# Kernel tuning notes

Hardware: AMD Instinct MI355X
Metric: run time of the kernel (lower is better)

The kernel has to match this reference:

```python
import jax, jax.numpy as jnp
import numpy as np

B, S, D, H, F = 4, 2048, 1024, 16, 4096
HD = D // H
EPS = 1e-5


def _xavier(key, shape, fan_in, fan_out):
    a = float(np.sqrt(6.0 / (fan_in + fan_out)))
    return jax.random.uniform(key, shape, jnp.float32, -a, a)


def setup_inputs() -> dict:
    key = jax.random.key(0)
    ks = jax.random.split(key, 8)
    x = jax.random.normal(ks[0], (B, S, D), jnp.float32)
    # torch xavier_uniform on (1,H,D,HD) uses fan_in=D, fan_out=HD
    Wq = _xavier(ks[1], (H, D, HD), D, HD)
    Wk = _xavier(ks[2], (H, D, HD), D, HD)
    Wv = _xavier(ks[3], (H, D, HD), D, HD)
    Wo = _xavier(ks[4], (D, D), D, D)
    w_in = _xavier(ks[5], (D, F), D, F)
    b_in = jnp.zeros((F,), jnp.float32)
    w_out = _xavier(ks[6], (F, D), F, D)
    b_out = jnp.zeros((D,), jnp.float32)
    g1 = jnp.ones((D,), jnp.float32)
    be1 = jnp.zeros((D,), jnp.float32)
    g2 = jnp.ones((D,), jnp.float32)
    be2 = jnp.zeros((D,), jnp.float32)
    return {"x": x, "Wq": Wq, "Wk": Wk, "Wv": Wv, "Wo": Wo,
            "g1": g1, "be1": be1, "w_in": w_in, "b_in": b_in,
            "w_out": w_out, "b_out": b_out, "g2": g2, "be2": be2}


def _layernorm(x, g, b):
    mu = jnp.mean(x, axis=-1, keepdims=True)
    var = jnp.mean(jnp.square(x - mu), axis=-1, keepdims=True)
    return (x - mu) * jax.lax.rsqrt(var + EPS) * g + b


def reference(x, Wq, Wk, Wv, Wo, g1, be1, w_in, b_in, w_out, b_out, g2, be2):
    b, s, d = x.shape
    h, _, hd = Wq.shape
    q = jnp.einsum('bsd,hde->bhse', x, Wq)
    k = jnp.einsum('bsd,hde->bhse', x, Wk)
    v = jnp.einsum('bsd,hde->bhse', x, Wv)
    scores = jnp.einsum('bhse,bhte->bhst', q, k) / jnp.sqrt(jnp.float32(hd))
    causal = jnp.triu(jnp.ones((s, s), bool), k=1)  # [S,S]
    scores = jnp.where(causal, -jnp.inf, scores)
    p = jax.nn.softmax(scores, axis=-1)
    attn = jnp.einsum('bhst,bhte->bhse', p, v)
    # torch .view on contiguous (B,H,S,hd) -> (B,S,H*hd): plain reshape (no transpose)
    attn = attn.reshape(b, s, h * hd)
    attn = attn @ Wo
    x = _layernorm(x + attn, g1, be1)
    ffn = jax.nn.relu(x @ w_in + b_in) @ w_out + b_out
    x = _layernorm(x + ffn, g2, be2)
    return x
```

## Files before the change

### kernel.cpp

```cpp
#include <hip/hip_runtime.h>
#include <hip/hip_bf16.h>

typedef __hip_bfloat16 bf16;

#define BB 4
#define SS 2048
#define DD 1024
#define HH 16
#define FF 4096
#define HD 64
#define LN_EPS 1e-5f
#define QSCALE 0.1803368801111204f

typedef __attribute__((ext_vector_type(8))) __bf16 bf16x8;
typedef __attribute__((ext_vector_type(8))) unsigned short u16x8;
typedef __attribute__((ext_vector_type(4))) float f32x4;

__device__ __forceinline__ float cvt(float v) { return v; }
__device__ __forceinline__ float cvt(bf16 v) { return __bfloat162float(v); }
__device__ __forceinline__ void stf(float* p, float v) { *p = v; }
__device__ __forceinline__ void stf(bf16* p, float v) { *p = __float2bfloat16(v); }

__device__ __forceinline__ unsigned short f2bf_rne(float x) {
    unsigned int u = __float_as_uint(x);
    unsigned int r = (u + 0x7fffu + ((u >> 16) & 1u)) >> 16;
    return (unsigned short)r;
}

__device__ __forceinline__ void async_cp16(const void* g, void* l) {
    __builtin_amdgcn_global_load_lds(
        (const __attribute__((address_space(1))) unsigned int*)g,
        (__attribute__((address_space(3))) unsigned int*)l, 16, 0, 0);
}

template <int N>
__device__ __forceinline__ void s_wait_vmcnt() {
    asm volatile("s_waitcnt vmcnt(%0)" ::"n"(N) : "memory");
    __builtin_amdgcn_sched_barrier(0);
}

__device__ __forceinline__ void sync_raw() {
    asm volatile("" ::: "memory");
    __builtin_amdgcn_s_barrier();
    asm volatile("" ::: "memory");
    __builtin_amdgcn_sched_barrier(0);
}

template <int EPI, int BW>
__device__ __forceinline__ void gemm_body(
        const bf16* __restrict__ A, const bf16* __restrict__ Bt,
        bf16* __restrict__ C, const float* __restrict__ bias,
        const bf16* __restrict__ resb,
        bf16* __restrict__ C2, bf16* __restrict__ C3,
        int M, int N, int K, float oscale) {
    __shared__ unsigned short As[128 * 64];
    __shared__ unsigned short Bs[128 * 64];

    const int tid = threadIdx.x;
    const int lane = tid & 63;
    const int w = tid >> 6;
    const int wm = w >> 1, wn = w & 1;

    const int gx = gridDim.x, gy = gridDim.y;
    const int id = blockIdx.y * gx + blockIdx.x;
    const int R = gy >> 3;
    const int k = id & 7;
    const int j = id >> 3;
    const int sbs = R * BW;
    const int sb = j / sbs;
    const int rem = j % sbs;
    const int by = k * R + rem / BW;
    const int bx = sb * BW + rem % BW;
    const int m0 = by * 128, n0 = bx * 128;

    int ff[4], fr[4], fg[4];
#pragma unroll
    for (int i = 0; i < 4; ++i) {
        ff[i] = tid + i * 256;
        fr[i] = ff[i] >> 3;
        fg[i] = (ff[i] & 7) ^ (fr[i] & 7);
    }

    f32x4 acc[4][4];
#pragma unroll
    for (int i = 0; i < 4; ++i)
#pragma unroll
        for (int j2 = 0; j2 < 4; ++j2) acc[i][j2] = (f32x4){0.f, 0.f, 0.f, 0.f};

    for (int k0 = 0; k0 < K; k0 += 64) {
        if (k0 > 0) __syncthreads();
#pragma unroll
        for (int i = 0; i < 4; ++i)
            async_cp16((const unsigned short*)A + (size_t)(m0 + fr[i]) * K + k0 + fg[i] * 8,
                       &As[ff[i] * 8]);
#pragma unroll
        for (int i = 0; i < 4; ++i)
            async_cp16((const unsigned short*)Bt + (size_t)(n0 + fr[i]) * K + k0 + fg[i] * 8,
                       &Bs[ff[i] * 8]);
        __syncthreads();

#pragma unroll
        for (int ks = 0; ks < 2; ++ks) {
            bf16x8 af[4], bfr[4];
#pragma unroll
            for (int i = 0; i < 4; ++i) {
                const int row = wm * 64 + i * 16 + (lane & 15);
                const int col = wn * 64 + i * 16 + (lane & 15);
                const int g = ks * 4 + (lane >> 4);
                af[i]  = *(const bf16x8*)&As[row * 64 + (g ^ (row & 7)) * 8];
                bfr[i] = *(const bf16x8*)&Bs[col * 64 + (g ^ (col & 7)) * 8];
            }
#pragma unroll
            for (int i = 0; i < 4; ++i)
#pragma unroll
                for (int j2 = 0; j2 < 4; ++j2)
                    acc[i][j2] = __builtin_amdgcn_mfma_f32_16x16x32_bf16(
                        af[i], bfr[j2], acc[i][j2], 0, 0, 0);
        }
    }

#pragma unroll
    for (int i = 0; i < 4; ++i) {
        const int mrow0 = m0 + wm * 64 + i * 16 + (lane >> 4) * 4;
#pragma unroll
        for (int j2 = 0; j2 < 4; ++j2) {
            const int n = n0 + wn * 64 + j2 * 16 + (lane & 15);
            if (EPI == 5) {
                const int reg = n >> 10;
                const int nn = n & 1023;
                if (reg == 0) {
#pragma unroll
                    for (int r = 0; r < 4; ++r)
                        stf((bf16*)C + (size_t)(mrow0 + r) * 1024 + nn, acc[i][j2][r] * oscale);
                } else if (reg == 1) {
#pragma unroll
                    for (int r = 0; r < 4; ++r)
                        stf(C2 + (size_t)(mrow0 + r) * 1024 + nn, acc[i][j2][r]);
                } else {
                    const int bb = mrow0 >> 11, s = mrow0 & 2047;
                    ushort4 pk;
                    pk.x = f2bf_rne(acc[i][j2][0]);
                    pk.y = f2bf_rne(acc[i][j2][1]);
                    pk.z = f2bf_rne(acc[i][j2][2]);
                    pk.w = f2bf_rne(acc[i][j2][3]);
                    *(ushort4*)((unsigned short*)C3 + ((size_t)bb * 1024 + nn) * SS + s) = pk;
                }
            } else {
#pragma unroll
                for (int r = 0; r < 4; ++r) {
                    const size_t idx = (size_t)(mrow0 + r) * N + n;
                    float v = acc[i][j2][r];
                    if (EPI == 2) { v += bias[n]; v = fmaxf(v, 0.0f); }
                    if (EPI == 6) v += bias[n] + cvt(resb[idx]);
                    if (EPI == 7) v += cvt(resb[idx]);
                    stf(&C[idx], v);
                }
            }
        }
    }
}

__launch_bounds__(256) __global__ void gemm_qkv(
        const bf16* __restrict__ A, const bf16* __restrict__ Bt, bf16* __restrict__ C,
        const float* __restrict__ bias, const bf16* __restrict__ resb,
        bf16* __restrict__ C2, bf16* __restrict__ C3, int M, int N, int K, float os) {
    gemm_body<5, 4>(A, Bt, C, bias, resb, C2, C3, M, N, K, os);
}
__launch_bounds__(256) __global__ void gemm_wo(
        const bf16* __restrict__ A, const bf16* __restrict__ Bt, bf16* __restrict__ C,
        const float* __restrict__ bias, const bf16* __restrict__ resb,
        bf16* __restrict__ C2, bf16* __restrict__ C3, int M, int N, int K, float os) {
    gemm_body<7, 8>(A, Bt, C, bias, resb, C2, C3, M, N, K, os);
}
__launch_bounds__(256) __global__ void gemm_ffn1(
        const bf16* __restrict__ A, const bf16* __restrict__ Bt, bf16* __restrict__ C,
        const float* __restrict__ bias, const bf16* __restrict__ resb,
        bf16* __restrict__ C2, bf16* __restrict__ C3, int M, int N, int K, float os) {
    gemm_body<2, 32>(A, Bt, C, bias, resb, C2, C3, M, N, K, os);
}
__launch_bounds__(256) __global__ void gemm_ffn2(
        const bf16* __restrict__ A, const bf16* __restrict__ Bt, bf16* __restrict__ C,
        const float* __restrict__ bias, const bf16* __restrict__ resb,
        bf16* __restrict__ C2, bf16* __restrict__ C3, int M, int N, int K, float os) {
    gemm_body<6, 8>(A, Bt, C, bias, resb, C2, C3, M, N, K, os);
}

__launch_bounds__(256)
__global__ void prep_kernel(const float* __restrict__ x,
                            const float* __restrict__ Wq, const float* __restrict__ Wk,
                            const float* __restrict__ Wv, const float* __restrict__ Wo,
                            const float* __restrict__ w_in, const float* __restrict__ w_out,
                            bf16* __restrict__ xb, bf16* __restrict__ WqkvT,
                            bf16* __restrict__ WoT, bf16* __restrict__ w_inT,
                            bf16* __restrict__ w_outT) {
    const int id = blockIdx.x;
    if (id < 8192) {
        const int i = id * 256 + threadIdx.x;
        const float4 v = ((const float4*)x)[i];
        ushort4 p;
        p.x = f2bf_rne(v.x); p.y = f2bf_rne(v.y); p.z = f2bf_rne(v.z); p.w = f2bf_rne(v.w);
        ((ushort4*)xb)[i] = p;
        return;
    }
    __shared__ float t[32][33];
    const int rem = id - 8192;
    const float* in;
    bf16* out;
    int R, C, bx, by;
    size_t in_o = 0, out_o = 0;
    if (rem < 3072) {
        const int z = rem >> 6, r2 = rem & 63;
        const int wi = z >> 4, head = z & 15;
        in = (wi == 0) ? Wq : (wi == 1) ? Wk : Wv;
        in_o = (size_t)head * DD * HD;
        out = WqkvT;
        out_o = (size_t)wi * DD * DD + (size_t)head * HD * DD;
        R = DD; C = HD;
        bx = (r2 & 1) * 32; by = (r2 >> 1) * 32;
    } else if (rem < 3072 + 1024) {
        const int r2 = rem - 3072;
        in = Wo; out = WoT; R = DD; C = DD;
        bx = (r2 & 31) * 32; by = (r2 >> 5) * 32;
    } else if (rem < 3072 + 1024 + 4096) {
        const int r2 = rem - 3072 - 1024;
        in = w_in; out = w_inT; R = DD; C = FF;
        bx = (r2 & 127) * 32; by = (r2 >> 7) * 32;
    } else {
        const int r2 = rem - 3072 - 1024 - 4096;
        in = w_out; out = w_outT; R = FF; C = DD;
        bx = (r2 & 31) * 32; by = (r2 >> 5) * 32;
    }
    const int tx = threadIdx.x & 31, ty = threadIdx.x >> 5;
#pragma unroll
    for (int i = 0; i < 32; i += 8)
        t[ty + i][tx] = in[in_o + (size_t)(by + ty + i) * C + bx + tx];
    __syncthreads();
#pragma unroll
    for (int i = 0; i < 32; i += 8)
        out[out_o + (size_t)(bx + ty + i) * R + by + tx] = __float2bfloat16(t[tx][ty + i]);
}

__launch_bounds__(256, 4)
__global__ void attn_mfma(const bf16* __restrict__ Q, const bf16* __restrict__ K,
                          const bf16* __restrict__ VT, bf16* __restrict__ O) {
    __shared__ unsigned short Ks[2][64 * 64];
    __shared__ unsigned short Vs[64 * 64];
    __shared__ unsigned short Ps[64 * 72];

    const int tid = threadIdx.x;
    const int lane = tid & 63;
    const int w = tid >> 6;
    const int ln = lane & 15;
    const int qd = lane >> 4;
    const int bh = blockIdx.x;
    const int b = bh >> 4;
    const int h = bh & 15;
    const int qi = 31 - blockIdx.y;
    const int q0 = qi * 64;

    bf16x8 aq[2];
    {
        const unsigned short* qp =
            (const unsigned short*)Q + ((size_t)b * SS + q0 + w * 16 + ln) * DD + h * HD;
        aq[0] = *(const bf16x8*)(qp + qd * 8);
        aq[1] = *(const bf16x8*)(qp + 32 + qd * 8);
    }

    int sf[2], sr[2], sg[2];
#pragma unroll
    for (int i = 0; i < 2; ++i) {
        sf[i] = tid + i * 256;
        sr[i] = sf[i] >> 3;
        sg[i] = (sf[i] & 7) ^ (sr[i] & 7);
    }
    const unsigned short* kbase = (const unsigned short*)K + (size_t)b * SS * DD + h * HD;
    const unsigned short* vbase = (const unsigned short*)VT + (size_t)(b * DD + h * HD) * SS;

    auto stageK = [&](int kt, int buf) {
        const int t0 = kt * 64;
#pragma unroll
        for (int i = 0; i < 2; ++i)
            async_cp16(kbase + (size_t)(t0 + sr[i]) * DD + sg[i] * 8, &Ks[buf][sf[i] * 8]);
    };
    auto stageV = [&](int kt) {
        const int t0 = kt * 64;
#pragma unroll
        for (int i = 0; i < 2; ++i)
            async_cp16(vbase + (size_t)sr[i] * SS + t0 + sg[i] * 8, &Vs[sf[i] * 8]);
    };

    f32x4 oacc[4];
#pragma unroll
    for (int e = 0; e < 4; ++e) oacc[e] = (f32x4){0.f, 0.f, 0.f, 0.f};
    float l_r[4] = {0.f, 0.f, 0.f, 0.f};

    stageK(0, 0);
    stageV(0);

    for (int kt = 0; kt <= qi; ++kt) {
        const int cur = kt & 1;
        if (kt > 0) stageV(kt);
        if (kt < qi) {
            stageK(kt + 1, cur ^ 1);
            s_wait_vmcnt<4>();
        } else {
            s_wait_vmcnt<2>();
        }
        sync_raw();

        f32x4 sfr[4];
#pragma unroll
        for (int ct = 0; ct < 4; ++ct) {
            const int row = ct * 16 + ln;
            const bf16x8 b0 = *(const bf16x8*)&Ks[cur][row * 64 + ((qd) ^ (row & 7)) * 8];
            const bf16x8 b1 = *(const bf16x8*)&Ks[cur][row * 64 + ((4 + qd) ^ (row & 7)) * 8];
            f32x4 t = __builtin_amdgcn_mfma_f32_16x16x32_bf16(
                aq[0], b0, (f32x4){0.f, 0.f, 0.f, 0.f}, 0, 0, 0);
            sfr[ct] = __builtin_amdgcn_mfma_f32_16x16x32_bf16(aq[1], b1, t, 0, 0, 0);
        }

        if (kt == qi) {
#pragma unroll
            for (int ct = 0; ct < 4; ++ct) {
                const int tg = kt * 64 + ct * 16 + ln;
#pragma unroll
                for (int r = 0; r < 4; ++r) {
                    const int qg = q0 + w * 16 + qd * 4 + r;
                    if (tg > qg) sfr[ct][r] = -1e30f;
                }
            }
        }

#pragma unroll
        for (int ct = 0; ct < 4; ++ct)
#pragma unroll
            for (int r = 0; r < 4; ++r)
                sfr[ct][r] = __builtin_amdgcn_exp2f(sfr[ct][r]);
#pragma unroll
        for (int r = 0; r < 4; ++r)
            l_r[r] += (sfr[0][r] + sfr[1][r]) + (sfr[2][r] + sfr[3][r]);

#pragma unroll
        for (int ct = 0; ct < 4; ++ct)
#pragma unroll
            for (int r = 0; r < 4; ++r)
                Ps[(w * 16 + qd * 4 + r) * 72 + ct * 16 + ln] = f2bf_rne(sfr[ct][r]);
        const bf16x8 ap0 = *(const bf16x8*)&Ps[(w * 16 + ln) * 72 + qd * 8];
        const bf16x8 ap1 = *(const bf16x8*)&Ps[(w * 16 + ln) * 72 + 32 + qd * 8];

        if (kt < qi) s_wait_vmcnt<2>();
        else         s_wait_vmcnt<0>();
        sync_raw();

#pragma unroll
        for (int et = 0; et < 4; ++et) {
            const int row = et * 16 + ln;
            const bf16x8 v0 = *(const bf16x8*)&Vs[row * 64 + ((qd) ^ (row & 7)) * 8];
            const bf16x8 v1 = *(const bf16x8*)&Vs[row * 64 + ((4 + qd) ^ (row & 7)) * 8];
            oacc[et] = __builtin_amdgcn_mfma_f32_16x16x32_bf16(ap0, v0, oacc[et], 0, 0, 0);
            oacc[et] = __builtin_amdgcn_mfma_f32_16x16x32_bf16(ap1, v1, oacc[et], 0, 0, 0);
        }

        asm volatile("s_waitcnt lgkmcnt(0)" ::: "memory");
        sync_raw();
    }

#pragma unroll
    for (int st = 1; st <= 8; st <<= 1)
#pragma unroll
        for (int r = 0; r < 4; ++r)
            l_r[r] += __shfl_xor(l_r[r], st);
    float linv[4];
#pragma unroll
    for (int r = 0; r < 4; ++r) linv[r] = 1.0f / l_r[r];
    unsigned short* ob = (unsigned short*)O + (size_t)bh * SS * HD;
#pragma unroll
    for (int et = 0; et < 4; ++et)
#pragma unroll
        for (int r = 0; r < 4; ++r) {
            const int qg = q0 + w * 16 + qd * 4 + r;
            ob[(size_t)qg * HD + et * 16 + ln] = f2bf_rne(oacc[et][r] * linv[r]);
        }
}

template <typename TIN, typename TOUT>
__launch_bounds__(256)
__global__ void ln_kernel(const TIN* __restrict__ X, TOUT* __restrict__ Y,
                          const float* __restrict__ g, const float* __restrict__ be) {
    const int row = blockIdx.x;
    const int tid = threadIdx.x;
    const int lane = tid & 63, w = tid >> 6;
    __shared__ float red[8];
    __shared__ float mv[2];

    float4 v;
    if (sizeof(TIN) == 4) {
        v = ((const float4*)((const float*)X + (size_t)row * DD))[tid];
    } else {
        const ushort4 u = ((const ushort4*)((const unsigned short*)X + (size_t)row * DD))[tid];
        v.x = __uint_as_float((unsigned)u.x << 16);
        v.y = __uint_as_float((unsigned)u.y << 16);
        v.z = __uint_as_float((unsigned)u.z << 16);
        v.w = __uint_as_float((unsigned)u.w << 16);
    }
    float s = (v.x + v.y) + (v.z + v.w);
    float q = (v.x * v.x + v.y * v.y) + (v.z * v.z + v.w * v.w);
#pragma unroll
    for (int st = 1; st < 64; st <<= 1) {
        s += __shfl_xor(s, st);
        q += __shfl_xor(q, st);
    }
    if (lane == 0) { red[w] = s; red[4 + w] = q; }
    __syncthreads();
    if (tid == 0) {
        const float ts = (red[0] + red[1]) + (red[2] + red[3]);
        const float tq = (red[4] + red[5]) + (red[6] + red[7]);
        const float mu = ts * (1.0f / DD);
        mv[0] = mu;
        mv[1] = rsqrtf(tq * (1.0f / DD) - mu * mu + LN_EPS);
    }
    __syncthreads();
    const float mu = mv[0], rs = mv[1];
    const float4 gg = ((const float4*)g)[tid];
    const float4 bb = ((const float4*)be)[tid];
    float o[4];
    o[0] = (v.x - mu) * rs * gg.x + bb.x;
    o[1] = (v.y - mu) * rs * gg.y + bb.y;
    o[2] = (v.z - mu) * rs * gg.z + bb.z;
    o[3] = (v.w - mu) * rs * gg.w + bb.w;
    if (sizeof(TOUT) == 4) {
        float4 of = {o[0], o[1], o[2], o[3]};
        ((float4*)((float*)Y + (size_t)row * DD))[tid] = of;
    } else {
        ushort4 p;
        p.x = f2bf_rne(o[0]); p.y = f2bf_rne(o[1]);
        p.z = f2bf_rne(o[2]); p.w = f2bf_rne(o[3]);
        ((ushort4*)((unsigned short*)Y + (size_t)row * DD))[tid] = p;
    }
}

extern "C" void kernel_launch(void* const* d_in, const int* in_sizes, int n_in,
                              void* d_out, int out_size, void* d_ws, size_t ws_size,
                              hipStream_t stream) {
    const float* x = (const float*)d_in[0];
    const float* Wq = (const float*)d_in[1];
    const float* Wk = (const float*)d_in[2];
    const float* Wv = (const float*)d_in[3];
    const float* Wo = (const float*)d_in[4];
    const float* g1 = (const float*)d_in[5];
    const float* be1 = (const float*)d_in[6];
    const float* w_in = (const float*)d_in[7];
    const float* b_in = (const float*)d_in[8];
    const float* w_out = (const float*)d_in[9];
    const float* b_out = (const float*)d_in[10];
    const float* g2 = (const float*)d_in[11];
    const float* be2 = (const float*)d_in[12];
    float* out = (float*)d_out;

    char* wsb = (char*)d_ws;
    const size_t MiB = 1u << 20;
    bf16* Qb = (bf16*)(wsb);
    bf16* Kb = (bf16*)(wsb + 16 * MiB);
    bf16* VT = (bf16*)(wsb + 32 * MiB);
    bf16* At = (bf16*)(wsb + 48 * MiB);
    bf16* xb = (bf16*)(wsb + 64 * MiB);
    bf16* X1b = (bf16*)(wsb + 80 * MiB);
    bf16* Hd = (bf16*)(wsb);
    bf16* X2b = (bf16*)(wsb + 64 * MiB);
    bf16* WqkvT = (bf16*)(wsb + 96 * MiB);
    bf16* WoT = (bf16*)(wsb + 102 * MiB);
    bf16* w_inT = (bf16*)(wsb + 104 * MiB);
    bf16* w_outT = (bf16*)(wsb + 112 * MiB);
    (void)ws_size;

    const int M = BB * SS;
    dim3 blk(256);

    prep_kernel<<<dim3(8192 + 3072 + 1024 + 4096 + 4096), blk, 0, stream>>>(
        x, Wq, Wk, Wv, Wo, w_in, w_out, xb, WqkvT, WoT, w_inT, w_outT);

    gemm_qkv<<<dim3(3 * DD / 128, M / 128), blk, 0, stream>>>(
        xb, WqkvT, Qb, nullptr, nullptr, Kb, VT, M, 3 * DD, DD, QSCALE);

    attn_mfma<<<dim3(BB * HH, SS / 64), blk, 0, stream>>>(Qb, Kb, VT, At);

    gemm_wo<<<dim3(DD / 128, M / 128), blk, 0, stream>>>(
        At, WoT, X1b, nullptr, xb, nullptr, nullptr, M, DD, DD, 1.0f);
    ln_kernel<bf16, bf16><<<dim3(M), blk, 0, stream>>>(X1b, X1b, g1, be1);

    gemm_ffn1<<<dim3(FF / 128, M / 128), blk, 0, stream>>>(
        X1b, w_inT, Hd, b_in, nullptr, nullptr, nullptr, M, FF, DD, 1.0f);

    gemm_ffn2<<<dim3(DD / 128, M / 128), blk, 0, stream>>>(
        Hd, w_outT, X2b, b_out, X1b, nullptr, nullptr, M, DD, FF, 1.0f);

    ln_kernel<bf16, float><<<dim3(M), blk, 0, stream>>>(X2b, out, g2, be2);
}
```

Baseline: 443.3 us.

## Enlarge attention query tile to 128 rows with 512-thread blocks

The attention kernel now processes 128 query rows per block using 8 waves (512 threads) instead of 64 rows with 4 waves. Each staged K/V tile in shared memory is reused by twice as many query rows, which halves the global K/V loads per query. Each thread now issues one async copy per tile instead of two, and the vmcnt waits and causal-mask bounds are adjusted to match. The trade-off is more LDS per block, fewer blocks in flight, and a coarser grid that may balance the causal triangle less evenly.

```diff
diff --git a/kernel.cpp b/kernel.cpp
--- a/kernel.cpp
+++ b/kernel.cpp
@@ -240,12 +240,12 @@
         out[out_o + (size_t)(bx + ty + i) * R + by + tx] = __float2bfloat16(t[tx][ty + i]);
 }
 
-__launch_bounds__(256, 4)
+__launch_bounds__(512, 6)
 __global__ void attn_mfma(const bf16* __restrict__ Q, const bf16* __restrict__ K,
                           const bf16* __restrict__ VT, bf16* __restrict__ O) {
     __shared__ unsigned short Ks[2][64 * 64];
     __shared__ unsigned short Vs[64 * 64];
-    __shared__ unsigned short Ps[64 * 72];
+    __shared__ unsigned short Ps[128 * 72];
 
     const int tid = threadIdx.x;
     const int lane = tid & 63;
@@ -255,8 +255,8 @@
     const int bh = blockIdx.x;
     const int b = bh >> 4;
     const int h = bh & 15;
-    const int qi = 31 - blockIdx.y;
-    const int q0 = qi * 64;
+    const int qi = 15 - blockIdx.y;
+    const int q0 = qi * 128;
 
     bf16x8 aq[2];
     {
@@ -266,27 +266,16 @@
         aq[1] = *(const bf16x8*)(qp + 32 + qd * 8);
     }
 
-    int sf[2], sr[2], sg[2];
-#pragma unroll
-    for (int i = 0; i < 2; ++i) {
-        sf[i] = tid + i * 256;
-        sr[i] = sf[i] >> 3;
-        sg[i] = (sf[i] & 7) ^ (sr[i] & 7);
-    }
+    const int sr = tid >> 3;
+    const int sg = (tid & 7) ^ (sr & 7);
     const unsigned short* kbase = (const unsigned short*)K + (size_t)b * SS * DD + h * HD;
     const unsigned short* vbase = (const unsigned short*)VT + (size_t)(b * DD + h * HD) * SS;
 
     auto stageK = [&](int kt, int buf) {
-        const int t0 = kt * 64;
-#pragma unroll
-        for (int i = 0; i < 2; ++i)
-            async_cp16(kbase + (size_t)(t0 + sr[i]) * DD + sg[i] * 8, &Ks[buf][sf[i] * 8]);
+        async_cp16(kbase + (size_t)(kt * 64 + sr) * DD + sg * 8, &Ks[buf][tid * 8]);
     };
     auto stageV = [&](int kt) {
-        const int t0 = kt * 64;
-#pragma unroll
-        for (int i = 0; i < 2; ++i)
-            async_cp16(vbase + (size_t)sr[i] * SS + t0 + sg[i] * 8, &Vs[sf[i] * 8]);
+        async_cp16(vbase + (size_t)sr * SS + kt * 64 + sg * 8, &Vs[tid * 8]);
     };
 
     f32x4 oacc[4];
@@ -294,17 +283,18 @@
     for (int e = 0; e < 4; ++e) oacc[e] = (f32x4){0.f, 0.f, 0.f, 0.f};
     float l_r[4] = {0.f, 0.f, 0.f, 0.f};
 
+    const int last = 2 * qi + 1;
     stageK(0, 0);
     stageV(0);
 
-    for (int kt = 0; kt <= qi; ++kt) {
+    for (int kt = 0; kt <= last; ++kt) {
         const int cur = kt & 1;
         if (kt > 0) stageV(kt);
-        if (kt < qi) {
+        if (kt < last) {
             stageK(kt + 1, cur ^ 1);
-            s_wait_vmcnt<4>();
+            s_wait_vmcnt<2>();
         } else {
-            s_wait_vmcnt<2>();
+            s_wait_vmcnt<1>();
         }
         sync_raw();
 
@@ -319,7 +309,7 @@
             sfr[ct] = __builtin_amdgcn_mfma_f32_16x16x32_bf16(aq[1], b1, t, 0, 0, 0);
         }
 
-        if (kt == qi) {
+        if (kt >= 2 * qi) {
 #pragma unroll
             for (int ct = 0; ct < 4; ++ct) {
                 const int tg = kt * 64 + ct * 16 + ln;
@@ -348,8 +338,8 @@
         const bf16x8 ap0 = *(const bf16x8*)&Ps[(w * 16 + ln) * 72 + qd * 8];
         const bf16x8 ap1 = *(const bf16x8*)&Ps[(w * 16 + ln) * 72 + 32 + qd * 8];
 
-        if (kt < qi) s_wait_vmcnt<2>();
-        else         s_wait_vmcnt<0>();
+        if (kt < last) s_wait_vmcnt<1>();
+        else           s_wait_vmcnt<0>();
         sync_raw();
 
 #pragma unroll
@@ -482,7 +472,7 @@
     gemm_qkv<<<dim3(3 * DD / 128, M / 128), blk, 0, stream>>>(
         xb, WqkvT, Qb, nullptr, nullptr, Kb, VT, M, 3 * DD, DD, QSCALE);
 
-    attn_mfma<<<dim3(BB * HH, SS / 64), blk, 0, stream>>>(Qb, Kb, VT, At);
+    attn_mfma<<<dim3(BB * HH, SS / 128), dim3(512), 0, stream>>>(Qb, Kb, VT, At);
 
     gemm_wo<<<dim3(DD / 128, M / 128), blk, 0, stream>>>(
         At, WoT, X1b, nullptr, xb, nullptr, nullptr, M, DD, DD, 1.0f);
```

Result: no change. 448.1 us (+1.1%).
